# Optimization experiments

Measured on AMD Instinct MI355X. Metric: run time of the kernel, lower is better.

## Reference

```python
import jax, jax.numpy as jnp
import numpy as np

NMS_THR = 0.5
PULL_W = 1.0
PUSH_W = 1.0
EPS = 1e-6


def bbox_overlaps(a, b):
    # a: [M,4], b: [N,4] in xyxy -> IoU [M,N]
    area_a = (a[:, 2] - a[:, 0]) * (a[:, 3] - a[:, 1])
    area_b = (b[:, 2] - b[:, 0]) * (b[:, 3] - b[:, 1])
    lt = jnp.maximum(a[:, None, :2], b[None, :, :2])
    rb = jnp.minimum(a[:, None, 2:], b[None, :, 2:])
    wh = jnp.clip(rb - lt, 0.0)
    inter = wh[..., 0] * wh[..., 1]
    return inter / (area_a[:, None] + area_b[None, :] - inter + 1e-12)


def single_nms_loss(gt_inds, gt_box, proposals):
    # gt_inds: [N] int (all >= 0), gt_box: [G,4], proposals: [N,5]
    N = proposals.shape[0]
    G = gt_box.shape[0]
    boxes = proposals[:, :4]
    scores = proposals[:, 4]
    sdet = jax.lax.stop_gradient(scores)
    # push_select=True: first argument of the proposal IoU is detached
    iou = bbox_overlaps(jax.lax.stop_gradient(boxes), boxes)  # [N,N]
    gt_iou = bbox_overlaps(gt_box, gt_box)                    # [G,G]
    gi = gt_inds.astype(jnp.int32)

    def step(carry, _):
        alive, rec, pull_s, push_s, pull_c, push_c = carry
        active = jnp.any(alive)
        i = jnp.argmax(jnp.where(alive, sdet, -jnp.inf)).astype(jnp.int32)
        g = gi[i]
        rec_g = rec[g]
        has_rec = rec_g >= 0
        max_idx = jnp.where(has_rec, rec_g, 0)
        max_s_iou = jnp.clip(iou[max_idx, i], EPS)
        # pull loss (fix_pull_reg=False, pull_score_up=False)
        pull = -jnp.log(1.0 - NMS_THR + max_s_iou) * sdet[i]
        rec = jnp.where(active & (~has_rec), rec.at[g].set(i), rec)
        alive2 = jnp.where(active, alive.at[i].set(False), alive)
        remaining = jnp.any(alive2)
        # torch code breaks BEFORE adding pull when no boxes remain
        do_pull = active & has_rec & remaining
        pull_s = pull_s + jnp.where(do_pull, pull, 0.0)
        pull_c = pull_c + jnp.where(active & has_rec, 1.0, 0.0)
        cur_iou = iou[i]                       # [N]
        overlap = alive2 & (cur_iou > NMS_THR)
        gt_row = gt_iou[g, gi]                 # [N]
        pmask = overlap & (gi != g) & (cur_iou > gt_row)
        safe_iou = jnp.where(pmask, cur_iou, 0.0)
        safe_sc = jnp.where(pmask, scores, 1.0)
        pvec = (-jnp.log(1.0 + NMS_THR - safe_iou) - jnp.log(safe_sc)) \
               * jax.lax.stop_gradient(safe_sc)
        cnt = jnp.sum(pmask)
        psum = jnp.sum(jnp.where(pmask, pvec, 0.0))
        push = jnp.where(cnt > 0, psum / jnp.maximum(cnt, 1).astype(pvec.dtype), 0.0)
        push_s = push_s + jnp.where(active, push, 0.0)
        push_c = push_c + jnp.where(active, cnt.astype(jnp.float32), 0.0)
        alive3 = alive2 & (~overlap)
        return (alive3, rec, pull_s, push_s, pull_c, push_c), None

    zero = jnp.float32(0.0)
    init = (jnp.ones(N, bool), -jnp.ones(G, jnp.int32), zero, zero, zero, zero)
    (_, _, pull_s, push_s, pull_c, push_c), _ = jax.lax.scan(step, init, None, length=N)
    return push_s / (push_c + EPS), pull_s / (pull_c + EPS)


def reference(gt_inds, anchor_gt_inds, gt_bboxes, proposal_list):
    # gt_inds is overwritten by anchor_gt_inds in the original code
    B = proposal_list.shape[0]
    push_t = jnp.float32(0.0)
    pull_t = jnp.float32(0.0)
    for b in range(B):
        push, pull = single_nms_loss(anchor_gt_inds[b], gt_bboxes[b], proposal_list[b])
        push_t = push_t + push
        pull_t = pull_t + pull
    return jnp.stack([push_t / B * PUSH_W, pull_t / B * PULL_W])


def setup_inputs() -> dict:
    key = jax.random.key(0)
    B, N, G = 2, 2048, 64
    ks = jax.random.split(key, 6)
    ctr = jax.random.uniform(ks[0], (B, N, 2)) * 512.0
    wh = jax.random.uniform(ks[1], (B, N, 2)) * 100.0 + 20.0
    boxes = jnp.concatenate([ctr - wh / 2, ctr + wh / 2], axis=-1)
    scores = jax.random.uniform(ks[2], (B, N, 1)) * 0.95 + 0.05
    proposal_list = jnp.concatenate([boxes, scores], axis=-1).astype(jnp.float32)
    gctr = jax.random.uniform(ks[3], (B, G, 2)) * 512.0
    gwh = jax.random.uniform(ks[4], (B, G, 2)) * 100.0 + 20.0
    gt_bboxes = jnp.concatenate([gctr - gwh / 2, gctr + gwh / 2], axis=-1).astype(jnp.float32)
    anchor_gt_inds = jax.random.randint(ks[5], (B, N), 0, G, dtype=jnp.int32)
    return {
        "gt_inds": anchor_gt_inds,
        "anchor_gt_inds": anchor_gt_inds,
        "gt_bboxes": gt_bboxes,
        "proposal_list": proposal_list,
    }
```

## Files before the change

### kernel.cpp

```cpp
#include <hip/hip_runtime.h>
#include <math.h>


#define NMS_THR 0.5f
#define EPS_F 1e-6f
#define NPAD 2048
#define NWORDS 32

__device__ __forceinline__ unsigned long long init_mask(int r, int N) {
    long base = (long)r * 64;
    if (base + 64 <= N) return ~0ULL;
    if (base >= N) return 0ULL;
    return (~0ULL) >> (64 - (int)(N - base));
}

__global__ __launch_bounds__(64, 1) void nms_loss_kernel(
    const int* __restrict__ gt_inds,
    const float* __restrict__ gt_bboxes,
    const float* __restrict__ proposals,
    float* __restrict__ out,
    int N, int G, float inv_B)
{
    const int b    = blockIdx.x;
    const int lane = threadIdx.x;

    __shared__ unsigned long long skey[NPAD];
    __shared__ float4 boxes_s[NPAD];
    __shared__ float  gtiou[64 * 64];
    float2* sgg_s = reinterpret_cast<float2*>(skey);

    const int*   gi_b   = gt_inds   + (size_t)b * N;
    const float* prop_b = proposals + (size_t)b * N * 5;
    const float* gtb    = gt_bboxes + (size_t)b * G * 4;

    for (int j = lane; j < NPAD; j += 64) {
        unsigned long long key;
        if (j < N) {
            float s = prop_b[(size_t)j * 5 + 4];
            key = ~(((unsigned long long)__float_as_uint(s) << 32)
                    | (unsigned long long)(0xffffffffu - (unsigned)j));
        } else {
            key = ~0ULL;
        }
        skey[j] = key;
    }
    __syncthreads();

    for (int k = 2; k <= NPAD; k <<= 1) {
        for (int jj = k >> 1; jj > 0; jj >>= 1) {
            for (int t = lane; t < NPAD; t += 64) {
                int l = t ^ jj;
                if (l > t) {
                    unsigned long long a = skey[t], c = skey[l];
                    bool up = ((t & k) == 0);
                    if ((a > c) == up) { skey[t] = c; skey[l] = a; }
                }
            }
            __syncthreads();
        }
    }

    unsigned idxs[NWORDS];
    #pragma unroll
    for (int w = 0; w < NWORDS; ++w) idxs[w] = (unsigned)skey[w * 64 + lane];
    __syncthreads();

    #pragma unroll
    for (int w = 0; w < NWORDS; ++w) {
        int sp = w * 64 + lane;
        if (sp < N) {
            unsigned idx = idxs[w];
            const float* pr = prop_b + (size_t)idx * 5;
            boxes_s[sp] = make_float4(pr[0], pr[1], pr[2], pr[3]);
            sgg_s[sp]   = make_float2(pr[4], __int_as_float(gi_b[idx]));
        } else {
            boxes_s[sp] = make_float4(0.f, 0.f, 0.f, 0.f);
            sgg_s[sp]   = make_float2(1.0f, __int_as_float(0));
        }
    }

    float4 gb = make_float4(0.f, 0.f, 0.f, 0.f);
    if (lane < G) {
        gb.x = gtb[lane * 4 + 0];
        gb.y = gtb[lane * 4 + 1];
        gb.z = gtb[lane * 4 + 2];
        gb.w = gtb[lane * 4 + 3];
    }
    float area_l = (gb.z - gb.x) * (gb.w - gb.y);
    for (int c = 0; c < G; ++c) {
        float cx1 = __shfl(gb.x, c), cy1 = __shfl(gb.y, c);
        float cx2 = __shfl(gb.z, c), cy2 = __shfl(gb.w, c);
        float area_c = (cx2 - cx1) * (cy2 - cy1);
        float ltx = fmaxf(gb.x, cx1), lty = fmaxf(gb.y, cy1);
        float rbx = fminf(gb.z, cx2), rby = fminf(gb.w, cy2);
        float w = fmaxf(rbx - ltx, 0.0f), h = fmaxf(rby - lty, 0.0f);
        float inter = w * h;
        if (lane < G)
            gtiou[lane * 64 + c] = inter / (area_l + area_c - inter + 1e-12f);
    }
    __syncthreads();

#define DECL_WORD(R) \
    float4 bx_##R = boxes_s[R * 64 + lane]; \
    float  ar_##R = (bx_##R.z - bx_##R.x) * (bx_##R.w - bx_##R.y); \
    float2 sg_##R = sgg_s[R * 64 + lane]; \
    float  sc_##R = sg_##R.x; \
    int    gi_##R = __float_as_int(sg_##R.y); \
    unsigned long long aw_##R = init_mask(R, N);

    DECL_WORD(0)  DECL_WORD(1)  DECL_WORD(2)  DECL_WORD(3)
    DECL_WORD(4)  DECL_WORD(5)  DECL_WORD(6)  DECL_WORD(7)
    DECL_WORD(8)  DECL_WORD(9)  DECL_WORD(10) DECL_WORD(11)
    DECL_WORD(12) DECL_WORD(13) DECL_WORD(14) DECL_WORD(15)
    DECL_WORD(16) DECL_WORD(17) DECL_WORD(18) DECL_WORD(19)
    DECL_WORD(20) DECL_WORD(21) DECL_WORD(22) DECL_WORD(23)
    DECL_WORD(24) DECL_WORD(25) DECL_WORD(26) DECL_WORD(27)
    DECL_WORD(28) DECL_WORD(29) DECL_WORD(30) DECL_WORD(31)
#undef DECL_WORD

    int   alive_count = N;
    int   rec_reg = -1;
    float rec_x = 0.f, rec_y = 0.f, rec_z = 0.f, rec_w = 0.f, rec_a = 0.f;
    float pull_s = 0.0f, push_s = 0.0f, pull_c = 0.0f, push_c = 0.0f;

    int p = (N > 0) ? 0 : -1;
    float4 nbi = make_float4(0.f, 0.f, 0.f, 0.f);
    float2 nsm = make_float2(1.0f, __int_as_float(0));
    if (p == 0) {
        aw_0 &= ~1ULL;
        nbi = boxes_s[0];
        nsm = sgg_s[0];
    }

    for (int step = 0; step < N && p >= 0; ++step) {
        const float4 bi = nbi;
        const float2 sm = nsm;
        const float  si = sm.x;
        const int    g  = __float_as_int(sm.y);
        const float  area_i = (bi.z - bi.x) * (bi.w - bi.y);

        const int  rec_g   = __shfl(rec_reg, g);
        const bool has_rec = rec_g >= 0;

        alive_count -= 1;
        const bool remaining = alive_count > 0;

        if (has_rec) {
            pull_c += 1.0f;
            if (remaining) {
                float brx = __shfl(rec_x, g), bry = __shfl(rec_y, g);
                float brz = __shfl(rec_z, g), brw = __shfl(rec_w, g);
                float area_r = __shfl(rec_a, g);
                float ltx = fmaxf(brx, bi.x), lty = fmaxf(bry, bi.y);
                float rbx = fminf(brz, bi.z), rby = fminf(brw, bi.w);
                float w = fmaxf(rbx - ltx, 0.0f), h = fmaxf(rby - lty, 0.0f);
                float inter = w * h;
                float iou = inter / (area_r + area_i - inter + 1e-12f);
                float msi = fmaxf(iou, EPS_F);
                pull_s += -logf(1.0f - NMS_THR + msi) * si;
            }
        } else {
            if (lane == g) {
                rec_reg = p;
                rec_x = bi.x; rec_y = bi.y; rec_z = bi.z; rec_w = bi.w;
                rec_a = area_i;
            }
        }

        float psum = 0.0f;
        int   pcnt = 0, killed = 0;
        int   next_p = -1;
        const float* __restrict__ gtrow = &gtiou[g * 64];

#define SCAN_WORD(R) \
        if (aw_##R != 0ULL) { \
            float ltx = fmaxf(bi.x, bx_##R.x), lty = fmaxf(bi.y, bx_##R.y); \
            float rbx = fminf(bi.z, bx_##R.z), rby = fminf(bi.w, bx_##R.w); \
            float w = fmaxf(rbx - ltx, 0.0f), h = fmaxf(rby - lty, 0.0f); \
            float inter = w * h; \
            float iou = inter / (area_i + ar_##R - inter + 1e-12f); \
            unsigned long long K = aw_##R & __ballot(iou > NMS_THR); \
            if (K) { \
                aw_##R &= ~K; \
                killed += __popcll(K); \
                unsigned long long E = \
                    K & __ballot((gi_##R != g) && (iou > gtrow[gi_##R])); \
                if (E) { \
                    pcnt += __popcll(E); \
                    bool elig = (E >> lane) & 1ULL; \
                    float pv = (-logf(1.0f + NMS_THR - iou) - logf(sc_##R)) \
                               * sc_##R; \
                    psum += elig ? pv : 0.0f; \
                } \
            } \
            if (next_p < 0 && aw_##R) { \
                int bp = __builtin_ctzll(aw_##R); \
                next_p = R * 64 + bp; \
                aw_##R &= ~(1ULL << bp); \
                nbi = boxes_s[next_p]; \
                nsm = sgg_s[next_p]; \
            } \
        }

        SCAN_WORD(0)  SCAN_WORD(1)  SCAN_WORD(2)  SCAN_WORD(3)
        SCAN_WORD(4)  SCAN_WORD(5)  SCAN_WORD(6)  SCAN_WORD(7)
        SCAN_WORD(8)  SCAN_WORD(9)  SCAN_WORD(10) SCAN_WORD(11)
        SCAN_WORD(12) SCAN_WORD(13) SCAN_WORD(14) SCAN_WORD(15)
        SCAN_WORD(16) SCAN_WORD(17) SCAN_WORD(18) SCAN_WORD(19)
        SCAN_WORD(20) SCAN_WORD(21) SCAN_WORD(22) SCAN_WORD(23)
        SCAN_WORD(24) SCAN_WORD(25) SCAN_WORD(26) SCAN_WORD(27)
        SCAN_WORD(28) SCAN_WORD(29) SCAN_WORD(30) SCAN_WORD(31)
#undef SCAN_WORD

        alive_count -= killed;
        if (pcnt > 0) {
            float ps = psum;
            for (int off = 32; off; off >>= 1) ps += __shfl_xor(ps, off);
            push_s += ps / (float)pcnt;
            push_c += (float)pcnt;
        }
        p = next_p;
    }

    float push_norm = push_s / (push_c + EPS_F);
    float pull_norm = pull_s / (pull_c + EPS_F);
    if (lane == 0) {
        atomicAdd(&out[0], push_norm * inv_B);
        atomicAdd(&out[1], pull_norm * inv_B);
    }
}

extern "C" void kernel_launch(void* const* d_in, const int* in_sizes, int n_in,
                              void* d_out, int out_size, void* d_ws, size_t ws_size,
                              hipStream_t stream) {
    const int B = 2;
    const int N = in_sizes[1] / B;
    const int G = in_sizes[2] / (B * 4);

    const int*   anchor_gt = (const int*)d_in[1];
    const float* gt_bboxes = (const float*)d_in[2];
    const float* proposals = (const float*)d_in[3];
    float* out = (float*)d_out;

    hipMemsetAsync(out, 0, 2 * sizeof(float), stream);
    nms_loss_kernel<<<B, 64, 0, stream>>>(anchor_gt, gt_bboxes, proposals,
                                          out, N, G, 1.0f / (float)B);
}
```

Measured before the change: 3.107 ms.

## Reload proposal boxes from LDS per scan and start scan at current word

Per-lane proposal boxes, areas, scores and gt indices are no longer held in 32 register sets. They are reloaded from shared memory inside the scan, which greatly cuts register pressure. The scan now enters a fall-through switch at the current box's 64-bit word, so words before it are skipped. The next candidate is picked with a branch-free min over per-word first-alive indices. Later words are scanned without the old all-dead early-out, and each step now pays extra LDS load latency.

```diff
diff --git a/kernel.cpp b/kernel.cpp
--- a/kernel.cpp
+++ b/kernel.cpp
@@ -6,6 +6,7 @@
 #define EPS_F 1e-6f
 #define NPAD 2048
 #define NWORDS 32
+#define INF_POS 0x7fffffff
 
 __device__ __forceinline__ unsigned long long init_mask(int r, int N) {
     long base = (long)r * 64;
@@ -100,23 +101,16 @@
     }
     __syncthreads();
 
-#define DECL_WORD(R) \
-    float4 bx_##R = boxes_s[R * 64 + lane]; \
-    float  ar_##R = (bx_##R.z - bx_##R.x) * (bx_##R.w - bx_##R.y); \
-    float2 sg_##R = sgg_s[R * 64 + lane]; \
-    float  sc_##R = sg_##R.x; \
-    int    gi_##R = __float_as_int(sg_##R.y); \
-    unsigned long long aw_##R = init_mask(R, N);
-
-    DECL_WORD(0)  DECL_WORD(1)  DECL_WORD(2)  DECL_WORD(3)
-    DECL_WORD(4)  DECL_WORD(5)  DECL_WORD(6)  DECL_WORD(7)
-    DECL_WORD(8)  DECL_WORD(9)  DECL_WORD(10) DECL_WORD(11)
-    DECL_WORD(12) DECL_WORD(13) DECL_WORD(14) DECL_WORD(15)
-    DECL_WORD(16) DECL_WORD(17) DECL_WORD(18) DECL_WORD(19)
-    DECL_WORD(20) DECL_WORD(21) DECL_WORD(22) DECL_WORD(23)
-    DECL_WORD(24) DECL_WORD(25) DECL_WORD(26) DECL_WORD(27)
-    DECL_WORD(28) DECL_WORD(29) DECL_WORD(30) DECL_WORD(31)
-#undef DECL_WORD
+#define DECL_AW(R) unsigned long long aw_##R = init_mask(R, N);
+    DECL_AW(0)  DECL_AW(1)  DECL_AW(2)  DECL_AW(3)
+    DECL_AW(4)  DECL_AW(5)  DECL_AW(6)  DECL_AW(7)
+    DECL_AW(8)  DECL_AW(9)  DECL_AW(10) DECL_AW(11)
+    DECL_AW(12) DECL_AW(13) DECL_AW(14) DECL_AW(15)
+    DECL_AW(16) DECL_AW(17) DECL_AW(18) DECL_AW(19)
+    DECL_AW(20) DECL_AW(21) DECL_AW(22) DECL_AW(23)
+    DECL_AW(24) DECL_AW(25) DECL_AW(26) DECL_AW(27)
+    DECL_AW(28) DECL_AW(29) DECL_AW(30) DECL_AW(31)
+#undef DECL_AW
 
     int   alive_count = N;
     int   rec_reg = -1;
@@ -127,7 +121,6 @@
     float4 nbi = make_float4(0.f, 0.f, 0.f, 0.f);
     float2 nsm = make_float2(1.0f, __int_as_float(0));
     if (p == 0) {
-        aw_0 &= ~1ULL;
         nbi = boxes_s[0];
         nsm = sgg_s[0];
     }
@@ -168,51 +161,85 @@
         }
 
         float psum = 0.0f;
-        int   pcnt = 0, killed = 0;
-        int   next_p = -1;
+        int   pcnt = 0;
+        int   killed_total = 0;
+        int   cand = INF_POS;
         const float* __restrict__ gtrow = &gtiou[g * 64];
 
 #define SCAN_WORD(R) \
-        if (aw_##R != 0ULL) { \
-            float ltx = fmaxf(bi.x, bx_##R.x), lty = fmaxf(bi.y, bx_##R.y); \
-            float rbx = fminf(bi.z, bx_##R.z), rby = fminf(bi.w, bx_##R.w); \
+        { \
+            float4 bx = boxes_s[R * 64 + lane]; \
+            float ar = (bx.z - bx.x) * (bx.w - bx.y); \
+            float ltx = fmaxf(bi.x, bx.x), lty = fmaxf(bi.y, bx.y); \
+            float rbx = fminf(bi.z, bx.z), rby = fminf(bi.w, bx.w); \
             float w = fmaxf(rbx - ltx, 0.0f), h = fmaxf(rby - lty, 0.0f); \
             float inter = w * h; \
-            float iou = inter / (area_i + ar_##R - inter + 1e-12f); \
+            float iou = inter / (area_i + ar - inter + 1e-12f); \
             unsigned long long K = aw_##R & __ballot(iou > NMS_THR); \
+            aw_##R &= ~K; \
+            killed_total += __popcll(K); \
             if (K) { \
-                aw_##R &= ~K; \
-                killed += __popcll(K); \
+                float2 sgj = sgg_s[R * 64 + lane]; \
+                int gj = __float_as_int(sgj.y); \
                 unsigned long long E = \
-                    K & __ballot((gi_##R != g) && (iou > gtrow[gi_##R])); \
+                    K & __ballot((gj != g) && (iou > gtrow[gj])); \
                 if (E) { \
                     pcnt += __popcll(E); \
                     bool elig = (E >> lane) & 1ULL; \
-                    float pv = (-logf(1.0f + NMS_THR - iou) - logf(sc_##R)) \
-                               * sc_##R; \
+                    float pv = (-logf(1.0f + NMS_THR - iou) - logf(sgj.x)) \
+                               * sgj.x; \
                     psum += elig ? pv : 0.0f; \
                 } \
             } \
-            if (next_p < 0 && aw_##R) { \
-                int bp = __builtin_ctzll(aw_##R); \
-                next_p = R * 64 + bp; \
-                aw_##R &= ~(1ULL << bp); \
-                nbi = boxes_s[next_p]; \
-                nsm = sgg_s[next_p]; \
-            } \
-        }
-
-        SCAN_WORD(0)  SCAN_WORD(1)  SCAN_WORD(2)  SCAN_WORD(3)
-        SCAN_WORD(4)  SCAN_WORD(5)  SCAN_WORD(6)  SCAN_WORD(7)
-        SCAN_WORD(8)  SCAN_WORD(9)  SCAN_WORD(10) SCAN_WORD(11)
-        SCAN_WORD(12) SCAN_WORD(13) SCAN_WORD(14) SCAN_WORD(15)
-        SCAN_WORD(16) SCAN_WORD(17) SCAN_WORD(18) SCAN_WORD(19)
-        SCAN_WORD(20) SCAN_WORD(21) SCAN_WORD(22) SCAN_WORD(23)
-        SCAN_WORD(24) SCAN_WORD(25) SCAN_WORD(26) SCAN_WORD(27)
-        SCAN_WORD(28) SCAN_WORD(29) SCAN_WORD(30) SCAN_WORD(31)
+            int c_ = aw_##R ? (R * 64 + (int)__builtin_ctzll(aw_##R)) \
+                            : INF_POS; \
+            cand = (c_ < cand) ? c_ : cand; \
+        }
+
+        switch (p >> 6) {
+        case 0:  SCAN_WORD(0)
+        case 1:  SCAN_WORD(1)
+        case 2:  SCAN_WORD(2)
+        case 3:  SCAN_WORD(3)
+        case 4:  SCAN_WORD(4)
+        case 5:  SCAN_WORD(5)
+        case 6:  SCAN_WORD(6)
+        case 7:  SCAN_WORD(7)
+        case 8:  SCAN_WORD(8)
+        case 9:  SCAN_WORD(9)
+        case 10: SCAN_WORD(10)
+        case 11: SCAN_WORD(11)
+        case 12: SCAN_WORD(12)
+        case 13: SCAN_WORD(13)
+        case 14: SCAN_WORD(14)
+        case 15: SCAN_WORD(15)
+        case 16: SCAN_WORD(16)
+        case 17: SCAN_WORD(17)
+        case 18: SCAN_WORD(18)
+        case 19: SCAN_WORD(19)
+        case 20: SCAN_WORD(20)
+        case 21: SCAN_WORD(21)
+        case 22: SCAN_WORD(22)
+        case 23: SCAN_WORD(23)
+        case 24: SCAN_WORD(24)
+        case 25: SCAN_WORD(25)
+        case 26: SCAN_WORD(26)
+        case 27: SCAN_WORD(27)
+        case 28: SCAN_WORD(28)
+        case 29: SCAN_WORD(29)
+        case 30: SCAN_WORD(30)
+        case 31: SCAN_WORD(31)
+        }
 #undef SCAN_WORD
 
-        alive_count -= killed;
+        const int next_p = (cand == INF_POS) ? -1 : cand;
+        if (next_p >= 0) {
+            nbi = boxes_s[next_p];
+            nsm = sgg_s[next_p];
+        }
+
+        killed_total -= 1;
+        alive_count  -= killed_total;
         if (pcnt > 0) {
             float ps = psum;
             for (int off = 32; off; off >>= 1) ps += __shfl_xor(ps, off);
```

Measured after the change: 3.925 ms. +26.3%, slower.
